# Performance work log

Hardware: AMD Instinct MI355X
Metric: run time of the kernel (lower is better)

Reference implementation:

```python
import jax, jax.numpy as jnp
import numpy as np

C = 768
H = 12
N = 257
B = 64
HID = 4 * C
EPS = 1e-5
SCALE = (C // H) ** -0.5


def layer_norm(x, g, b):
    m = x.mean(-1, keepdims=True)
    v = ((x - m) ** 2).mean(-1, keepdims=True)
    return (x - m) * jax.lax.rsqrt(v + EPS) * g + b


def qkv_split(x, qkv_w):
    # x: [B,N,C]; qkv_w: [3C,C] (torch Linear layout)
    qkv = jnp.einsum('bnc,oc->bno', x, qkv_w)  # [B,N,3C]
    qkv = qkv.reshape(x.shape[0], x.shape[1], 3, H, C // H)
    qkv = jnp.transpose(qkv, (2, 0, 3, 1, 4))  # [3,B,H,N,hd]
    return qkv[0], qkv[1], qkv[2]


def self_attn(x, qkv_w, proj_w, proj_b):
    q, k, v = qkv_split(x, qkv_w)
    attn = jax.nn.softmax(jnp.einsum('bhnd,bhmd->bhnm', q, k) * SCALE, axis=-1)
    o = jnp.einsum('bhnm,bhmd->bhnd', attn, v)
    o = jnp.transpose(o, (0, 2, 1, 3)).reshape(x.shape)
    return jnp.einsum('bnc,oc->bno', o, proj_w) + proj_b


def cross_attn(x, y, qkv_w, proj_w, proj_b):
    qx, _, _ = qkv_split(x, qkv_w)
    _, ky, vy = qkv_split(y, qkv_w)
    attn = jax.nn.softmax(jnp.einsum('bhnd,bhmd->bhnm', qx, ky) * SCALE, axis=-1)
    o = jnp.einsum('bhnm,bhmd->bhnd', attn, vy)
    o = jnp.transpose(o, (0, 2, 1, 3)).reshape(x.shape)
    return jnp.einsum('bnc,oc->bno', o, proj_w) + proj_b, attn.sum(1)  # [B,N,N]


def mlp(x, w1, b1, w2, b2):
    h = jax.nn.gelu(jnp.einsum('bnc,hc->bnh', x, w1) + b1, approximate=False)
    return jnp.einsum('bnh,ch->bnc', h, w2) + b2


def arf(x):
    tmp = (jnp.exp(x) - jnp.exp(-x)) / (jnp.exp(x) + jnp.exp(-x - 4.0))
    return jnp.where(tmp < 0, jnp.zeros_like(x), tmp)


def setup_inputs() -> dict:
    key = jax.random.key(0)
    ks = jax.random.split(key, 16)
    s = 0.02
    return {
        'src': jax.random.normal(ks[0], (B, N, C), jnp.float32),
        'tgt': jax.random.normal(ks[1], (B, N, C), jnp.float32),
        'sattn_qkv_w': jax.random.normal(ks[2], (3 * C, C), jnp.float32) * s,
        'sattn_proj_w': jax.random.normal(ks[3], (C, C), jnp.float32) * s,
        'sattn_proj_b': jnp.zeros((C,), jnp.float32),
        'cattn_qkv_w': jax.random.normal(ks[4], (3 * C, C), jnp.float32) * s,
        'cattn_proj_w': jax.random.normal(ks[5], (C, C), jnp.float32) * s,
        'cattn_proj_b': jnp.zeros((C,), jnp.float32),
        'norm1_g': jnp.ones((C,), jnp.float32),
        'norm1_b': jnp.zeros((C,), jnp.float32),
        'norm2_g': jnp.ones((C,), jnp.float32),
        'norm2_b': jnp.zeros((C,), jnp.float32),
        'fc1_w': jax.random.normal(ks[6], (HID, C), jnp.float32) * s,
        'fc1_b': jnp.zeros((HID,), jnp.float32),
        'fc2_w': jax.random.normal(ks[7], (C, HID), jnp.float32) * s,
        'fc2_b': jnp.zeros((C,), jnp.float32),
        'sa_weight': jnp.ones((1, 1, C), jnp.float32),
        'pos_embed': jax.random.normal(ks[8], (1, N, C), jnp.float32) * s,
    }


def reference(src, tgt, sattn_qkv_w, sattn_proj_w, sattn_proj_b,
              cattn_qkv_w, cattn_proj_w, cattn_proj_b,
              norm1_g, norm1_b, norm2_g, norm2_b,
              fc1_w, fc1_b, fc2_w, fc2_b, sa_weight, pos_embed):
    src = src + pos_embed
    srct = self_attn(layer_norm(src, norm1_g, norm1_b), sattn_qkv_w, sattn_proj_w, sattn_proj_b)
    tgtt = self_attn(layer_norm(tgt, norm1_g, norm1_b), sattn_qkv_w, sattn_proj_w, sattn_proj_b)
    src = src + srct
    tgt = tgt + tgtt
    src = src + mlp(layer_norm(srct, norm2_g, norm2_b), fc1_w, fc1_b, fc2_w, fc2_b)
    tgt = tgt + mlp(layer_norm(tgtt, norm2_g, norm2_b), fc1_w, fc1_b, fc2_w, fc2_b)
    srct, attn_src = cross_attn(layer_norm(src, norm1_g, norm1_b),
                                layer_norm(tgt, norm1_g, norm1_b),
                                cattn_qkv_w, cattn_proj_w, cattn_proj_b)
    srct = arf(srct)
    src = src + srct
    src = src + mlp(layer_norm(srct, norm2_g, norm2_b), fc1_w, fc1_b, fc2_w, fc2_b)
    attm_out = attn_src[:, 1:, 1:]
    # heat gate (no grad through attn_src here)
    heat = jax.lax.stop_gradient(attn_src)
    heat = heat.mean(1).reshape(attn_src.shape[0], N, 1)  # [B,N,1]
    gate = jax.nn.sigmoid(heat)
    tgt = tgt + tgt * sa_weight * gate
    return src, tgt, attm_out
```

## Files before the change

### kernel.cpp

```cpp
#include <hip/hip_runtime.h>

#define N_SEQ  257
#define BATCH  64
#define CDIM   768
#define HEADS  12
#define HDIM   64
#define HIDDEN 3072
#define MROWS  (BATCH * N_SEQ)

typedef unsigned short u16;
typedef unsigned int   u32;
typedef __bf16 bf16x8 __attribute__((ext_vector_type(8)));
typedef float  f32x4  __attribute__((ext_vector_type(4)));

__device__ __forceinline__ float b2f(u16 u) { u32 x = ((u32)u) << 16; return __uint_as_float(x); }
__device__ __forceinline__ u16   f2b(float f) {
    u32 x = __float_as_uint(f);
    u32 r = (x + 0x7fffu + ((x >> 16) & 1u)) >> 16;
    return (u16)r;
}
__device__ __forceinline__ float ldf(const float x) { return x; }
__device__ __forceinline__ float ldf(const u16 x)   { return b2f(x); }

__device__ __forceinline__ float geluf(float x) { return 0.5f * x * (1.f + erff(x * 0.70710678118654752f)); }
__device__ __forceinline__ float arff(float x) {
    if (x <= 0.f) return 0.f;
    float a = expf(-2.f * x);
    float c = expf(-2.f * x - 4.f);
    return (1.f - a) / (1.f + c);
}

template<bool MAXOP>
__device__ __forceinline__ float block_red(float v, float* scratch, int tid) {
#pragma unroll
    for (int off = 32; off > 0; off >>= 1) {
        float o = __shfl_down(v, off, 64);
        v = MAXOP ? fmaxf(v, o) : v + o;
    }
    if ((tid & 63) == 0) scratch[tid >> 6] = v;
    __syncthreads();
    float r = MAXOP ? fmaxf(fmaxf(scratch[0], scratch[1]), fmaxf(scratch[2], scratch[3]))
                    : (scratch[0] + scratch[1]) + (scratch[2] + scratch[3]);
    __syncthreads();
    return r;
}

__global__ void detect_kernel(const u16* __restrict__ g1, u32* __restrict__ flag)
{
    if (threadIdx.x == 0 && blockIdx.x == 0) *flag = (g1[0] == 0x3F80u) ? 1u : 0u;
}

__global__ __launch_bounds__(256)
void conv_kernel(const void* __restrict__ s, u16* __restrict__ d, int n,
                 const u32* __restrict__ flag)
{
    const int i = blockIdx.x * 256 + threadIdx.x;
    if (i >= n) return;
    if (*flag) d[i] = ((const u16*)s)[i];
    else       d[i] = f2b(((const float*)s)[i]);
}

#define LDSW 40

template<int EP>
__global__ __launch_bounds__(256)
void gemm_kernel(const u16* __restrict__ A, const u16* __restrict__ W,
                 const u16* __restrict__ bias, u16* __restrict__ Co,
                 float* __restrict__ resid, int M, int Ncols, int K)
{
    __shared__ __align__(16) u16 sA[128 * LDSW];
    __shared__ __align__(16) u16 sB[128 * LDSW];
    const int tid  = threadIdx.x;
    const int bm0  = blockIdx.y * 128;
    const int n0   = blockIdx.x * 128;
    const int lane = tid & 63, wave = tid >> 6;
    const int wm = (wave >> 1) << 6;
    const int wn = (wave & 1) << 6;
    const int r16 = lane & 15, quad = lane >> 4;

    f32x4 acc[4][4] = {};

    for (int k0 = 0; k0 < K; k0 += 32) {
        __syncthreads();
#pragma unroll
        for (int it = 0; it < 2; ++it) {
            int c2  = tid + (it << 8);
            int row = c2 >> 2;
            int col = (c2 & 3) << 3;
            int gm  = bm0 + row; if (gm >= M) gm = M - 1;
            *reinterpret_cast<uint4*>(&sA[row * LDSW + col]) =
                *reinterpret_cast<const uint4*>(A + (size_t)gm * K + k0 + col);
            *reinterpret_cast<uint4*>(&sB[row * LDSW + col]) =
                *reinterpret_cast<const uint4*>(W + (size_t)(n0 + row) * K + k0 + col);
        }
        __syncthreads();

        bf16x8 af[4], bfr[4];
#pragma unroll
        for (int i = 0; i < 4; ++i) {
            af[i]  = *reinterpret_cast<const bf16x8*>(&sA[(wm + i * 16 + r16) * LDSW + quad * 8]);
            bfr[i] = *reinterpret_cast<const bf16x8*>(&sB[(wn + i * 16 + r16) * LDSW + quad * 8]);
        }
#pragma unroll
        for (int i = 0; i < 4; ++i)
#pragma unroll
            for (int j = 0; j < 4; ++j)
                acc[i][j] = __builtin_amdgcn_mfma_f32_16x16x32_bf16(af[i], bfr[j], acc[i][j], 0, 0, 0);
    }

#pragma unroll
    for (int i = 0; i < 4; ++i) {
#pragma unroll
        for (int j = 0; j < 4; ++j) {
            const int gn = n0 + wn + j * 16 + r16;
            const float bv = bias ? b2f(bias[gn]) : 0.f;
#pragma unroll
            for (int r = 0; r < 4; ++r) {
                const int gm = bm0 + wm + i * 16 + quad * 4 + r;
                if (gm < M) {
                    float v = acc[i][j][r] + bv;
                    const size_t oidx = (size_t)gm * Ncols + gn;
                    if (EP == 1) v = geluf(v);
                    if (EP == 3) v = arff(v);
                    if (EP == 0 || EP == 1) Co[oidx] = f2b(v);
                    if (EP == 2 || EP == 3) { Co[oidx] = f2b(v); resid[oidx] += v; }
                    if (EP == 4) resid[oidx] += v;
                }
            }
        }
    }
}

template<typename T>
__global__ __launch_bounds__(256)
void ln_kernel(const T* __restrict__ x, const u16* __restrict__ g,
               const u16* __restrict__ be, u16* __restrict__ y)
{
    __shared__ float scratch[4];
    const int row = blockIdx.x, tid = threadIdx.x;
    const size_t base = (size_t)row * CDIM;
    float v[3];
#pragma unroll
    for (int i = 0; i < 3; ++i) v[i] = ldf(x[base + tid + i * 256]);
    float mean = block_red<false>(v[0] + v[1] + v[2], scratch, tid) * (1.f / 768.f);
    float d0 = v[0] - mean, d1 = v[1] - mean, d2 = v[2] - mean;
    float var = block_red<false>(d0 * d0 + d1 * d1 + d2 * d2, scratch, tid) * (1.f / 768.f);
    float rstd = rsqrtf(var + 1e-5f);
#pragma unroll
    for (int i = 0; i < 3; ++i) {
        int c = tid + i * 256;
        y[base + c] = f2b((v[i] - mean) * rstd * b2f(g[c]) + b2f(be[c]));
    }
}

__global__ __launch_bounds__(256)
void attn_flash_kernel(const u16* __restrict__ Q, int qs,
                       const u16* __restrict__ Kp, int ks,
                       const u16* __restrict__ Vp, int vs,
                       u16* __restrict__ O, float* __restrict__ asum)
{
    __shared__ __align__(16) u16 Qs[64 * 72];
    __shared__ __align__(16) u16 Ks[64 * 72];
    __shared__ __align__(16) u16 Ps[64 * 72];
    __shared__ __align__(16) u16 Vt[64 * 328];
    const int tid = threadIdx.x;
    const int n0 = blockIdx.x * 64;
    const int h  = blockIdx.y, b = blockIdx.z;
    const int lane = tid & 63, w = tid >> 6;
    const int r16 = lane & 15, quad = lane >> 4;

    {
        int id = tid;
#pragma unroll
        for (int it = 0; it < 2; ++it, id += 256) {
            int row = id >> 3, dc = (id & 7) << 3;
            int gn = n0 + row; if (gn > 256) gn = 256;
            *reinterpret_cast<uint4*>(&Qs[row * 72 + dc]) =
                *reinterpret_cast<const uint4*>(Q + (size_t)(b * N_SEQ + gn) * qs + h * HDIM + dc);
        }
    }
    for (int id = tid; id < 320 * 8; id += 256) {
        int m = id >> 3, dc = (id & 7) << 3;
        int gm = m > 256 ? 256 : m;
        uint4 v4 = *reinterpret_cast<const uint4*>(Vp + (size_t)(b * N_SEQ + gm) * vs + h * HDIM + dc);
        const u16* vv = reinterpret_cast<const u16*>(&v4);
#pragma unroll
        for (int j = 0; j < 8; ++j) Vt[(dc + j) * 328 + m] = vv[j];
    }
    __syncthreads();

    const bf16x8 af0 = *reinterpret_cast<const bf16x8*>(&Qs[(w * 16 + r16) * 72 + quad * 8]);
    const bf16x8 af1 = *reinterpret_cast<const bf16x8*>(&Qs[(w * 16 + r16) * 72 + 32 + quad * 8]);

    f32x4 O4[4];
#pragma unroll
    for (int s = 0; s < 4; ++s) O4[s] = (f32x4){0.f, 0.f, 0.f, 0.f};
    float m_[4] = { -3.0e38f, -3.0e38f, -3.0e38f, -3.0e38f };
    float l_[4] = { 0.f, 0.f, 0.f, 0.f };

    for (int kt = 0; kt < 5; ++kt) {
        __syncthreads();
        {
            int id = tid;
#pragma unroll
            for (int it = 0; it < 2; ++it, id += 256) {
                int row = id >> 3, dc = (id & 7) << 3;
                int gm = kt * 64 + row; if (gm > 256) gm = 256;
                *reinterpret_cast<uint4*>(&Ks[row * 72 + dc]) =
                    *reinterpret_cast<const uint4*>(Kp + (size_t)(b * N_SEQ + gm) * ks + h * HDIM + dc);
            }
        }
        __syncthreads();

        f32x4 s4[4];
#pragma unroll
        for (int s = 0; s < 4; ++s) s4[s] = (f32x4){0.f, 0.f, 0.f, 0.f};
#pragma unroll
        for (int s = 0; s < 4; ++s) {
            bf16x8 b0 = *reinterpret_cast<const bf16x8*>(&Ks[(s * 16 + r16) * 72 + quad * 8]);
            bf16x8 b1 = *reinterpret_cast<const bf16x8*>(&Ks[(s * 16 + r16) * 72 + 32 + quad * 8]);
            s4[s] = __builtin_amdgcn_mfma_f32_16x16x32_bf16(af0, b0, s4[s], 0, 0, 0);
            s4[s] = __builtin_amdgcn_mfma_f32_16x16x32_bf16(af1, b1, s4[s], 0, 0, 0);
        }

#pragma unroll
        for (int s = 0; s < 4; ++s)
#pragma unroll
            for (int r = 0; r < 4; ++r) {
                float v = s4[s][r] * 0.125f;
                if (kt == 4 && (s * 16 + r16) >= 1) v = -3.0e38f;
                s4[s][r] = v;
            }

#pragma unroll
        for (int r = 0; r < 4; ++r) {
            float tmax = fmaxf(fmaxf(s4[0][r], s4[1][r]), fmaxf(s4[2][r], s4[3][r]));
#pragma unroll
            for (int msk = 1; msk < 16; msk <<= 1) tmax = fmaxf(tmax, __shfl_xor(tmax, msk, 64));
            float mn = fmaxf(m_[r], tmax);
            float corr = __expf(m_[r] - mn);
            m_[r] = mn;
            float rs = 0.f;
#pragma unroll
            for (int s = 0; s < 4; ++s) {
                float p = __expf(s4[s][r] - mn);
                s4[s][r] = p; rs += p;
            }
#pragma unroll
            for (int msk = 1; msk < 16; msk <<= 1) rs += __shfl_xor(rs, msk, 64);
            l_[r] = l_[r] * corr + rs;
#pragma unroll
            for (int s = 0; s < 4; ++s) O4[s][r] *= corr;
        }

#pragma unroll
        for (int ts = 0; ts < 4; ++ts)
#pragma unroll
            for (int r = 0; r < 4; ++r)
                Ps[(w * 16 + quad * 4 + r) * 72 + ts * 16 + r16] = f2b(s4[ts][r]);
        bf16x8 p0 = *reinterpret_cast<const bf16x8*>(&Ps[(w * 16 + r16) * 72 + quad * 8]);
        bf16x8 p1 = *reinterpret_cast<const bf16x8*>(&Ps[(w * 16 + r16) * 72 + 32 + quad * 8]);
#pragma unroll
        for (int s = 0; s < 4; ++s) {
            bf16x8 v0 = *reinterpret_cast<const bf16x8*>(&Vt[(s * 16 + r16) * 328 + kt * 64 + quad * 8]);
            bf16x8 v1 = *reinterpret_cast<const bf16x8*>(&Vt[(s * 16 + r16) * 328 + kt * 64 + 32 + quad * 8]);
            O4[s] = __builtin_amdgcn_mfma_f32_16x16x32_bf16(p0, v0, O4[s], 0, 0, 0);
            O4[s] = __builtin_amdgcn_mfma_f32_16x16x32_bf16(p1, v1, O4[s], 0, 0, 0);
        }
    }

    float inv[4];
#pragma unroll
    for (int r = 0; r < 4; ++r) inv[r] = 1.f / l_[r];

#pragma unroll
    for (int s = 0; s < 4; ++s) {
#pragma unroll
        for (int r = 0; r < 4; ++r) {
            const int n = n0 + w * 16 + quad * 4 + r;
            if (n < N_SEQ)
                O[(size_t)(b * N_SEQ + n) * CDIM + h * HDIM + s * 16 + r16] = f2b(O4[s][r] * inv[r]);
        }
    }

    if (asum) {
        for (int kt = 0; kt < 5; ++kt) {
            __syncthreads();
            {
                int id = tid;
#pragma unroll
                for (int it = 0; it < 2; ++it, id += 256) {
                    int row = id >> 3, dc = (id & 7) << 3;
                    int gm = kt * 64 + row; if (gm > 256) gm = 256;
                    *reinterpret_cast<uint4*>(&Ks[row * 72 + dc]) =
                        *reinterpret_cast<const uint4*>(Kp + (size_t)(b * N_SEQ + gm) * ks + h * HDIM + dc);
                }
            }
            __syncthreads();

            f32x4 s4[4];
#pragma unroll
            for (int s = 0; s < 4; ++s) s4[s] = (f32x4){0.f, 0.f, 0.f, 0.f};
#pragma unroll
            for (int s = 0; s < 4; ++s) {
                bf16x8 b0 = *reinterpret_cast<const bf16x8*>(&Ks[(s * 16 + r16) * 72 + quad * 8]);
                bf16x8 b1 = *reinterpret_cast<const bf16x8*>(&Ks[(s * 16 + r16) * 72 + 32 + quad * 8]);
                s4[s] = __builtin_amdgcn_mfma_f32_16x16x32_bf16(af0, b0, s4[s], 0, 0, 0);
                s4[s] = __builtin_amdgcn_mfma_f32_16x16x32_bf16(af1, b1, s4[s], 0, 0, 0);
            }
#pragma unroll
            for (int s = 0; s < 4; ++s)
#pragma unroll
                for (int r = 0; r < 4; ++r) {
                    const int key = kt * 64 + s * 16 + r16;
                    const int n = n0 + w * 16 + quad * 4 + r;
                    if (key < N_SEQ && n < N_SEQ) {
                        float p = __expf(s4[s][r] * 0.125f - m_[r]) * inv[r];
                        atomicAdd(&asum[((size_t)b * N_SEQ + n) * N_SEQ + key], p);
                    }
                }
        }
    }
}

__global__ __launch_bounds__(256)
void init_kernel(const void* __restrict__ src, const void* __restrict__ tgt,
                 const void* __restrict__ pos, float* __restrict__ sa,
                 float* __restrict__ ta, const u32* __restrict__ flag)
{
    const u32 i = blockIdx.x * 256 + threadIdx.x;
    const u32 p = i % (u32)(N_SEQ * CDIM);
    float sv, tv, pv;
    if (*flag) {
        sv = b2f(((const u16*)src)[i]); tv = b2f(((const u16*)tgt)[i]); pv = b2f(((const u16*)pos)[p]);
    } else {
        sv = ((const float*)src)[i];    tv = ((const float*)tgt)[i];    pv = ((const float*)pos)[p];
    }
    sa[i] = sv + pv;
    ta[i] = tv;
}

__global__ __launch_bounds__(256)
void zero_kernel(float* __restrict__ p, int n)
{
    const int i = blockIdx.x * 256 + threadIdx.x;
    if (i < n) p[i] = 0.f;
}

__global__ __launch_bounds__(256)
void gate_kernel(const float* __restrict__ asum, float* __restrict__ gate)
{
    const int b = blockIdx.x;
    for (int m = threadIdx.x; m < N_SEQ; m += 256) {
        float s = 0.f;
        for (int q = 0; q < N_SEQ; ++q)
            s += asum[((size_t)b * N_SEQ + q) * N_SEQ + m];
        s *= (1.f / 257.f);
        gate[b * N_SEQ + m] = 1.f / (1.f + expf(-s));
    }
}

__global__ __launch_bounds__(256)
void final_kernel(const float* __restrict__ sa, const float* __restrict__ ta,
                  const u16* __restrict__ saw, const float* __restrict__ gate,
                  void* __restrict__ osrc_v, const u32* __restrict__ flag)
{
    const u32 i = blockIdx.x * 256 + threadIdx.x;
    const int c  = i % CDIM;
    const int bn = i / CDIM;
    const float so = sa[i];
    const float to = ta[i] * (1.f + b2f(saw[c]) * gate[bn]);
    const size_t BNC = (size_t)MROWS * CDIM;
    if (*flag) {
        u16* o = (u16*)osrc_v;
        o[i] = f2b(so); o[BNC + i] = f2b(to);
    } else {
        float* o = (float*)osrc_v;
        o[i] = so; o[BNC + i] = to;
    }
}

__global__ __launch_bounds__(256)
void attm_kernel(const float* __restrict__ asum, void* __restrict__ out_v,
                 const u32* __restrict__ flag)
{
    const u32 i = blockIdx.x * 256 + threadIdx.x;
    const int b = i >> 16;
    const int r = (i >> 8) & 255;
    const int c = i & 255;
    const float v = asum[((size_t)b * N_SEQ + (r + 1)) * N_SEQ + (c + 1)];
    const size_t off = 2 * (size_t)MROWS * CDIM;
    if (*flag) ((u16*)out_v)[off + i] = f2b(v);
    else       ((float*)out_v)[off + i] = v;
}

extern "C" void kernel_launch(void* const* d_in, const int* in_sizes, int n_in,
                              void* d_out, int out_size, void* d_ws, size_t ws_size,
                              hipStream_t stream)
{
    const void* src    = d_in[0];
    const void* tgt    = d_in[1];
    const void* pos    = d_in[17];

    const int M = MROWS;
    const size_t BNC = (size_t)M * CDIM;

    float* SA   = (float*)d_ws;
    float* TA   = SA + BNC;
    u16*   Cb   = (u16*)(TA + BNC);
    u16*   Db   = Cb + BNC;
    u16*   Eb   = Db + BNC;
    float* ASUM = (float*)(Eb + 4 * BNC);
    float* GATE = ASUM + (size_t)BATCH * N_SEQ * N_SEQ;
    u16*   WB   = (u16*)(GATE + (size_t)BATCH * N_SEQ);
    u16* w_sqkv   = WB;
    u16* w_sproj  = w_sqkv  + 1769472;
    u16* w_sprojb = w_sproj + 589824;
    u16* w_cqkv   = w_sprojb + 768;
    u16* w_cproj  = w_cqkv  + 1769472;
    u16* w_cprojb = w_cproj + 589824;
    u16* w_g1     = w_cprojb + 768;
    u16* w_b1     = w_g1 + 768;
    u16* w_g2     = w_b1 + 768;
    u16* w_b2     = w_g2 + 768;
    u16* w_fc1    = w_b2 + 768;
    u16* w_fc1b   = w_fc1 + 2359296;
    u16* w_fc2    = w_fc1b + 3072;
    u16* w_fc2b   = w_fc2 + 2359296;
    u16* w_saw    = w_fc2b + 768;
    u32* FLAG     = (u32*)(w_saw + 768);
    if (ws_size < (size_t)((char*)(FLAG + 4) - (char*)d_ws)) return;

    const dim3 blk(256, 1, 1);
    const int gM = (M + 127) / 128;
    const dim3 agrid(5, HEADS, BATCH);

    detect_kernel<<<dim3(1), dim3(64), 0, stream>>>((const u16*)d_in[8], FLAG);

    auto conv = [&](int idx, u16* dst, int n) {
        conv_kernel<<<dim3((n + 255) / 256), blk, 0, stream>>>(d_in[idx], dst, n, FLAG);
    };
    conv(2,  w_sqkv,   1769472);
    conv(3,  w_sproj,  589824);
    conv(4,  w_sprojb, 768);
    conv(5,  w_cqkv,   1769472);
    conv(6,  w_cproj,  589824);
    conv(7,  w_cprojb, 768);
    conv(8,  w_g1,     768);
    conv(9,  w_b1,     768);
    conv(10, w_g2,     768);
    conv(11, w_b2,     768);
    conv(12, w_fc1,    2359296);
    conv(13, w_fc1b,   3072);
    conv(14, w_fc2,    2359296);
    conv(15, w_fc2b,   768);
    conv(16, w_saw,    768);

    init_kernel<<<dim3((u32)(BNC / 256)), blk, 0, stream>>>(src, tgt, pos, SA, TA, FLAG);

    ln_kernel<float><<<dim3(M), blk, 0, stream>>>(SA, w_g1, w_b1, Db);
    gemm_kernel<0><<<dim3(2304 / 128, gM), blk, 0, stream>>>(Db, w_sqkv, nullptr, Eb, nullptr, M, 2304, CDIM);
    attn_flash_kernel<<<agrid, blk, 0, stream>>>(Eb, 2304, Eb + 768, 2304, Eb + 1536, 2304, Db, nullptr);
    gemm_kernel<2><<<dim3(6, gM), blk, 0, stream>>>(Db, w_sproj, w_sprojb, Cb, SA, M, CDIM, CDIM);
    ln_kernel<u16><<<dim3(M), blk, 0, stream>>>(Cb, w_g2, w_b2, Db);
    gemm_kernel<1><<<dim3(HIDDEN / 128, gM), blk, 0, stream>>>(Db, w_fc1, w_fc1b, Eb, nullptr, M, HIDDEN, CDIM);
    gemm_kernel<4><<<dim3(6, gM), blk, 0, stream>>>(Eb, w_fc2, w_fc2b, nullptr, SA, M, CDIM, HIDDEN);

    ln_kernel<float><<<dim3(M), blk, 0, stream>>>(TA, w_g1, w_b1, Db);
    gemm_kernel<0><<<dim3(2304 / 128, gM), blk, 0, stream>>>(Db, w_sqkv, nullptr, Eb, nullptr, M, 2304, CDIM);
    attn_flash_kernel<<<agrid, blk, 0, stream>>>(Eb, 2304, Eb + 768, 2304, Eb + 1536, 2304, Db, nullptr);
    gemm_kernel<2><<<dim3(6, gM), blk, 0, stream>>>(Db, w_sproj, w_sprojb, Cb, TA, M, CDIM, CDIM);
    ln_kernel<u16><<<dim3(M), blk, 0, stream>>>(Cb, w_g2, w_b2, Db);
    gemm_kernel<1><<<dim3(HIDDEN / 128, gM), blk, 0, stream>>>(Db, w_fc1, w_fc1b, Eb, nullptr, M, HIDDEN, CDIM);
    gemm_kernel<4><<<dim3(6, gM), blk, 0, stream>>>(Eb, w_fc2, w_fc2b, nullptr, TA, M, CDIM, HIDDEN);

    u16* EKV = Eb + BNC;
    ln_kernel<float><<<dim3(M), blk, 0, stream>>>(SA, w_g1, w_b1, Db);
    gemm_kernel<0><<<dim3(6, gM), blk, 0, stream>>>(Db, w_cqkv, nullptr, Eb, nullptr, M, CDIM, CDIM);
    ln_kernel<float><<<dim3(M), blk, 0, stream>>>(TA, w_g1, w_b1, Db);
    gemm_kernel<0><<<dim3(12, gM), blk, 0, stream>>>(Db, w_cqkv + 768 * 768, nullptr, EKV, nullptr, M, 1536, CDIM);
    const int asum_n = BATCH * N_SEQ * N_SEQ;
    zero_kernel<<<dim3((asum_n + 255) / 256), blk, 0, stream>>>(ASUM, asum_n);
    attn_flash_kernel<<<agrid, blk, 0, stream>>>(Eb, 768, EKV, 1536, EKV + 768, 1536, Db, ASUM);
    gemm_kernel<3><<<dim3(6, gM), blk, 0, stream>>>(Db, w_cproj, w_cprojb, Cb, SA, M, CDIM, CDIM);
    ln_kernel<u16><<<dim3(M), blk, 0, stream>>>(Cb, w_g2, w_b2, Db);
    gemm_kernel<1><<<dim3(HIDDEN / 128, gM), blk, 0, stream>>>(Db, w_fc1, w_fc1b, Eb, nullptr, M, HIDDEN, CDIM);
    gemm_kernel<4><<<dim3(6, gM), blk, 0, stream>>>(Eb, w_fc2, w_fc2b, nullptr, SA, M, CDIM, HIDDEN);

    gate_kernel<<<dim3(BATCH), blk, 0, stream>>>(ASUM, GATE);
    final_kernel<<<dim3((u32)(BNC / 256)), blk, 0, stream>>>(SA, TA, w_saw, GATE, d_out, FLAG);
    attm_kernel<<<dim3(BATCH * 256 * 256 / 256), blk, 0, stream>>>(ASUM, d_out, FLAG);
}
```

Before: 2.735 ms.

## Load Q/K fragments directly from global, double-buffer swizzled V tiles in attention

```diff
diff --git a/kernel.cpp b/kernel.cpp
--- a/kernel.cpp
+++ b/kernel.cpp
@@ -153,44 +153,41 @@
     }
 }
 
-__global__ __launch_bounds__(256)
+__global__ __launch_bounds__(256, 4)
 void attn_flash_kernel(const u16* __restrict__ Q, int qs,
                        const u16* __restrict__ Kp, int ks,
                        const u16* __restrict__ Vp, int vs,
                        u16* __restrict__ O, float* __restrict__ asum)
 {
-    __shared__ __align__(16) u16 Qs[64 * 72];
-    __shared__ __align__(16) u16 Ks[64 * 72];
+    __shared__ __align__(16) u16 Vt[2][64 * 64];
     __shared__ __align__(16) u16 Ps[64 * 72];
-    __shared__ __align__(16) u16 Vt[64 * 328];
     const int tid = threadIdx.x;
     const int n0 = blockIdx.x * 64;
     const int h  = blockIdx.y, b = blockIdx.z;
     const int lane = tid & 63, w = tid >> 6;
     const int r16 = lane & 15, quad = lane >> 4;
 
-    {
-        int id = tid;
-#pragma unroll
-        for (int it = 0; it < 2; ++it, id += 256) {
-            int row = id >> 3, dc = (id & 7) << 3;
-            int gn = n0 + row; if (gn > 256) gn = 256;
-            *reinterpret_cast<uint4*>(&Qs[row * 72 + dc]) =
-                *reinterpret_cast<const uint4*>(Q + (size_t)(b * N_SEQ + gn) * qs + h * HDIM + dc);
-        }
-    }
-    for (int id = tid; id < 320 * 8; id += 256) {
-        int m = id >> 3, dc = (id & 7) << 3;
-        int gm = m > 256 ? 256 : m;
-        uint4 v4 = *reinterpret_cast<const uint4*>(Vp + (size_t)(b * N_SEQ + gm) * vs + h * HDIM + dc);
-        const u16* vv = reinterpret_cast<const u16*>(&v4);
-#pragma unroll
-        for (int j = 0; j < 8; ++j) Vt[(dc + j) * 328 + m] = vv[j];
-    }
-    __syncthreads();
-
-    const bf16x8 af0 = *reinterpret_cast<const bf16x8*>(&Qs[(w * 16 + r16) * 72 + quad * 8]);
-    const bf16x8 af1 = *reinterpret_cast<const bf16x8*>(&Qs[(w * 16 + r16) * 72 + 32 + quad * 8]);
+    int qrow = n0 + w * 16 + r16; if (qrow > 256) qrow = 256;
+    const u16* qp = Q + (size_t)(b * N_SEQ + qrow) * qs + h * HDIM + quad * 8;
+    const bf16x8 af0 = *reinterpret_cast<const bf16x8*>(qp);
+    const bf16x8 af1 = *reinterpret_cast<const bf16x8*>(qp + 32);
+
+    auto stageV = [&](int kt, int buf) {
+#pragma unroll
+        for (int it = 0; it < 2; ++it) {
+            int id  = tid + (it << 8);
+            int key = id & 63;
+            int dc  = ((id >> 6) & 7) << 3;
+            int gm  = kt * 64 + key; if (gm > 256) gm = 256;
+            uint4 v4 = *reinterpret_cast<const uint4*>(Vp + (size_t)(b * N_SEQ + gm) * vs + h * HDIM + dc);
+            const u16* vv = reinterpret_cast<const u16*>(&v4);
+#pragma unroll
+            for (int j = 0; j < 8; ++j) {
+                int d = dc + j;
+                Vt[buf][d * 64 + (key ^ ((d & 7) << 3))] = vv[j];
+            }
+        }
+    };
 
     f32x4 O4[4];
 #pragma unroll
@@ -198,27 +195,21 @@
     float m_[4] = { -3.0e38f, -3.0e38f, -3.0e38f, -3.0e38f };
     float l_[4] = { 0.f, 0.f, 0.f, 0.f };
 
+    stageV(0, 0);
+    __syncthreads();
+
     for (int kt = 0; kt < 5; ++kt) {
-        __syncthreads();
-        {
-            int id = tid;
-#pragma unroll
-            for (int it = 0; it < 2; ++it, id += 256) {
-                int row = id >> 3, dc = (id & 7) << 3;
-                int gm = kt * 64 + row; if (gm > 256) gm = 256;
-                *reinterpret_cast<uint4*>(&Ks[row * 72 + dc]) =
-                    *reinterpret_cast<const uint4*>(Kp + (size_t)(b * N_SEQ + gm) * ks + h * HDIM + dc);
-            }
-        }
-        __syncthreads();
+        if (kt < 4) stageV(kt + 1, (kt + 1) & 1);
 
         f32x4 s4[4];
 #pragma unroll
         for (int s = 0; s < 4; ++s) s4[s] = (f32x4){0.f, 0.f, 0.f, 0.f};
 #pragma unroll
         for (int s = 0; s < 4; ++s) {
-            bf16x8 b0 = *reinterpret_cast<const bf16x8*>(&Ks[(s * 16 + r16) * 72 + quad * 8]);
-            bf16x8 b1 = *reinterpret_cast<const bf16x8*>(&Ks[(s * 16 + r16) * 72 + 32 + quad * 8]);
+            int krow = kt * 64 + s * 16 + r16; if (krow > 256) krow = 256;
+            const u16* kp = Kp + (size_t)(b * N_SEQ + krow) * ks + h * HDIM + quad * 8;
+            bf16x8 b0 = *reinterpret_cast<const bf16x8*>(kp);
+            bf16x8 b1 = *reinterpret_cast<const bf16x8*>(kp + 32);
             s4[s] = __builtin_amdgcn_mfma_f32_16x16x32_bf16(af0, b0, s4[s], 0, 0, 0);
             s4[s] = __builtin_amdgcn_mfma_f32_16x16x32_bf16(af1, b1, s4[s], 0, 0, 0);
         }
@@ -262,11 +253,15 @@
         bf16x8 p1 = *reinterpret_cast<const bf16x8*>(&Ps[(w * 16 + r16) * 72 + 32 + quad * 8]);
 #pragma unroll
         for (int s = 0; s < 4; ++s) {
-            bf16x8 v0 = *reinterpret_cast<const bf16x8*>(&Vt[(s * 16 + r16) * 328 + kt * 64 + quad * 8]);
-            bf16x8 v1 = *reinterpret_cast<const bf16x8*>(&Vt[(s * 16 + r16) * 328 + kt * 64 + 32 + quad * 8]);
+            const int d0 = s * 16 + r16;
+            const int sw = (d0 & 7) << 3;
+            bf16x8 v0 = *reinterpret_cast<const bf16x8*>(&Vt[kt & 1][d0 * 64 + ((quad * 8) ^ sw)]);
+            bf16x8 v1 = *reinterpret_cast<const bf16x8*>(&Vt[kt & 1][d0 * 64 + ((32 + quad * 8) ^ sw)]);
             O4[s] = __builtin_amdgcn_mfma_f32_16x16x32_bf16(p0, v0, O4[s], 0, 0, 0);
             O4[s] = __builtin_amdgcn_mfma_f32_16x16x32_bf16(p1, v1, O4[s], 0, 0, 0);
         }
+
+        __syncthreads();
     }
 
     float inv[4];
@@ -285,26 +280,15 @@
 
     if (asum) {
         for (int kt = 0; kt < 5; ++kt) {
-            __syncthreads();
-            {
-                int id = tid;
-#pragma unroll
-                for (int it = 0; it < 2; ++it, id += 256) {
-                    int row = id >> 3, dc = (id & 7) << 3;
-                    int gm = kt * 64 + row; if (gm > 256) gm = 256;
-                    *reinterpret_cast<uint4*>(&Ks[row * 72 + dc]) =
-                        *reinterpret_cast<const uint4*>(Kp + (size_t)(b * N_SEQ + gm) * ks + h * HDIM + dc);
-                }
-            }
-            __syncthreads();
-
             f32x4 s4[4];
 #pragma unroll
             for (int s = 0; s < 4; ++s) s4[s] = (f32x4){0.f, 0.f, 0.f, 0.f};
 #pragma unroll
             for (int s = 0; s < 4; ++s) {
-                bf16x8 b0 = *reinterpret_cast<const bf16x8*>(&Ks[(s * 16 + r16) * 72 + quad * 8]);
-                bf16x8 b1 = *reinterpret_cast<const bf16x8*>(&Ks[(s * 16 + r16) * 72 + 32 + quad * 8]);
+                int krow = kt * 64 + s * 16 + r16; if (krow > 256) krow = 256;
+                const u16* kp = Kp + (size_t)(b * N_SEQ + krow) * ks + h * HDIM + quad * 8;
+                bf16x8 b0 = *reinterpret_cast<const bf16x8*>(kp);
+                bf16x8 b1 = *reinterpret_cast<const bf16x8*>(kp + 32);
                 s4[s] = __builtin_amdgcn_mfma_f32_16x16x32_bf16(af0, b0, s4[s], 0, 0, 0);
                 s4[s] = __builtin_amdgcn_mfma_f32_16x16x32_bf16(af1, b1, s4[s], 0, 0, 0);
             }
```

Measured after the change: 2.692 ms. No clear change (-1.6%).
